# Optimization experiments

Measured on AMD Instinct MI355X. Metric: run time of the kernel, lower is better.

## Reference

```python
import jax, jax.numpy as jnp
from jax import lax
import numpy as np

RADIUS = 1
DILATION = 2
NUM_BINS = 16  # DualSimilarityLoss uses num_bins=16
ALPHA = 5.0
BETA = 0.1
NOISE = 1e-4


def _avg_pool2(x):
    b, c, h, w = x.shape
    return x.reshape(b, c, h // 2, 2, w // 2, 2).mean(axis=(3, 5))


def _conv_rep(x, k, pad):
    # replicate-pad then VALID conv, NCHW / OIHW
    xp = jnp.pad(x, ((0, 0), (0, 0), (pad, pad), (pad, pad)), mode='edge')
    return lax.conv_general_dilated(xp, k, (1, 1), 'VALID',
                                    dimension_numbers=('NCHW', 'OIHW', 'NCHW'))


def _upsample_align_corners(x, H, W):
    # bilinear, align_corners=True (matches F.interpolate(..., align_corners=True))
    b, c, h, w = x.shape

    def coords(n_out, n_in):
        pos = jnp.arange(n_out, dtype=x.dtype) * ((n_in - 1) / (n_out - 1))
        i0 = jnp.clip(jnp.floor(pos).astype(jnp.int32), 0, n_in - 2)
        return i0, pos - i0.astype(x.dtype)

    y0, fy = coords(H, h)
    x0, fx = coords(W, w)
    rows = x[:, :, y0, :] * (1.0 - fy)[None, None, :, None] \
         + x[:, :, y0 + 1, :] * fy[None, None, :, None]
    out = rows[:, :, :, x0] * (1.0 - fx) + rows[:, :, :, x0 + 1] * fx
    return out


def _compute_mind(img, key):
    B, _, H, W = img.shape
    img = _avg_pool2(img)                      # (B,1,H/2,W/2)
    img = img + NOISE * jax.random.normal(key, img.shape, img.dtype)
    h, w = img.shape[2], img.shape[3]
    pad = RADIUS * DILATION                    # 2
    k = 2 * RADIUS + 1                         # 3
    ones_k = jnp.ones((1, 1, k, k), img.dtype)
    padded = jnp.pad(img, ((0, 0), (0, 0), (pad, pad), (pad, pad)), mode='edge')
    patch_mean = lax.conv_general_dilated(padded, ones_k, (1, 1), 'VALID',
                                          dimension_numbers=('NCHW', 'OIHW', 'NCHW')) / (k * k)
    patch_mean = jnp.pad(patch_mean, ((0, 0), (0, 0), (pad, pad), (pad, pad)), mode='edge')
    c = pad
    center = padded[:, :, c:c + h, c:c + w]
    variance = (center - patch_mean[:, :, c:c + h, c:c + w]) ** 2
    variance = _conv_rep(variance, ones_k, RADIUS) / (k * k)
    variance = jnp.maximum(variance, 1e-4)
    descs = []
    for i in range(-RADIUS, RADIUS + 1):
        for j in range(-RADIUS, RADIUS + 1):
            if i == 0 and j == 0:
                continue
            dx, dy = i * DILATION, j * DILATION
            off = padded[:, :, c + dy:c + dy + h, c + dx:c + dx + w]
            diff = jnp.clip((center - off) ** 2 / (variance * 2 + 1e-6), 0.0, 50.0)
            descs.append(diff)
    m = jnp.exp(-jnp.concatenate(descs, axis=1))          # (B,8,h,w)
    m = m / (m.sum(axis=1, keepdims=True) + 1e-8)
    m = jnp.where(jnp.isnan(m), 0.0, m)
    if (h, w) != (H, W):
        m = _upsample_align_corners(m, H, W)
    return m


def _nmi_loss(x, y, kx, ky):
    B = x.shape[0]
    x = x[:, :, ::2, ::2]
    y = y[:, :, ::2, ::2]
    x = x + NOISE * jax.random.normal(kx, x.shape, x.dtype)
    y = y + NOISE * jax.random.normal(ky, y.shape, y.dtype)
    xf = jnp.clip((x.reshape(B, -1) + 1.0) / 2.0, 0.001, 0.999)
    yf = jnp.clip((y.reshape(B, -1) + 1.0) / 2.0, 0.001, 0.999)
    grid = jnp.linspace(0.0, 1.0, NUM_BINS + 1)
    xb = jnp.clip(jnp.searchsorted(grid, xf, side='left') - 1, 0, NUM_BINS - 1)
    yb = jnp.clip(jnp.searchsorted(grid, yf, side='left') - 1, 0, NUM_BINS - 1)
    idx = xb * NUM_BINS + yb                               # (B,N)
    hist = jnp.zeros((B, NUM_BINS * NUM_BINS), jnp.float32)
    hist = hist.at[jnp.arange(B)[:, None], idx].add(1.0)
    hist = hist.reshape(B, NUM_BINS, NUM_BINS)
    hist = hist / (hist.sum(axis=(1, 2), keepdims=True) + 1e-10)
    xh = hist.sum(axis=2)
    yh = hist.sum(axis=1)
    eps = 1e-5
    hist = hist + eps
    xh = xh + eps
    yh = yh + eps
    mi = jnp.sum(hist * (jnp.log(hist) - jnp.log(xh[:, :, None] * yh[:, None, :])), axis=(1, 2))
    hx = -jnp.sum(xh * jnp.log(xh), axis=1)
    hy = -jnp.sum(yh * jnp.log(yh), axis=1)
    se = hx + hy
    nmi = jnp.where(se < 1e-10, 0.0, 2.0 * mi / se)
    nmi = jnp.clip(nmi, -1.0, 1.0)
    return -jnp.clip(nmi.mean(), -1.0, 1.0)


def _reg_loss(flow, ku, kv):
    sx = jnp.array([[-1, 0, 1], [-2, 0, 2], [-1, 0, 1]], jnp.float32).reshape(1, 1, 3, 3)
    sy = jnp.array([[-1, -2, -1], [0, 0, 0], [1, 2, 1]], jnp.float32).reshape(1, 1, 3, 3)
    lp = jnp.array([[0, 1, 0], [1, -4, 1], [0, 1, 0]], jnp.float32).reshape(1, 1, 3, 3)
    f = _avg_pool2(flow)
    u = f[:, 0:1] + NOISE * jax.random.normal(ku, f[:, 0:1].shape, f.dtype)
    v = f[:, 1:2] + NOISE * jax.random.normal(kv, f[:, 1:2].shape, f.dtype)
    grad_mag = _conv_rep(u, sx, 1) ** 2 + _conv_rep(u, sy, 1) ** 2 \
             + _conv_rep(v, sx, 1) ** 2 + _conv_rep(v, sy, 1) ** 2
    lap_mag = _conv_rep(u, lp, 1) ** 2 + _conv_rep(v, lp, 1) ** 2
    return jnp.clip(grad_mag, 0.0, 100.0).mean() + jnp.clip(lap_mag, 0.0, 100.0).mean()


def _total_loss(fixed, moved, flow):
    fixed = jnp.where(jnp.isnan(fixed), 0.0, fixed)
    moved = jnp.where(jnp.isnan(moved), 0.0, moved)
    flow = jnp.where(jnp.isnan(flow), 0.0, flow)
    ks = jax.random.split(jax.random.key(42), 6)
    mi = _nmi_loss(fixed, moved, ks[0], ks[1])
    mx = _compute_mind(fixed, ks[2])
    my = _compute_mind(moved, ks[3])
    d = jnp.abs(mx - my)
    mind = jnp.where(jnp.isnan(d), 0.0, d).mean()
    reg = _reg_loss(flow, ks[4], ks[5])
    return mi + ALPHA * mind + BETA * reg


def setup_inputs() -> dict:
    key = jax.random.key(0)
    k1, k2, k3 = jax.random.split(key, 3)
    B, H, W = 8, 512, 512
    return {
        'fixed': jax.random.normal(k1, (B, 1, H, W), jnp.float32),
        'moved': jax.random.normal(k2, (B, 1, H, W), jnp.float32),
        'flow': jax.random.normal(k3, (B, 2, H, W), jnp.float32),
    }


def reference(fixed, moved, flow):
    return _total_loss(fixed, moved, flow)
```

## Files before the change

### kernel.cpp

```cpp
#include <hip/hip_runtime.h>
#include <cmath>

#define BATCH 8
#define HF 512
#define WF 512
#define HS 256
#define WS 256
#define PLANE_S (HS * WS)
#define PLANE_F (HF * WF)

#define NMIND_BLOCKS 512
#define NREG_BLOCKS  128

#define OFF_HISTP 0
#define OFF_PMIND (512 * 1024)
#define OFF_PGRAD (OFF_PMIND + NMIND_BLOCKS * 8)
#define OFF_PLAP  (OFF_PGRAD + NREG_BLOCKS * 8)
#define OFF_NMI   (OFF_PLAP + NREG_BLOCKS * 8)

#define IMG_R 39
#define IMG_S 41
#define T_R 36
#define T_S 37
#define V_R 34
#define V_S 35

__device__ __forceinline__ int clampi(int v, int lo, int hi) {
    return v < lo ? lo : (v > hi ? hi : v);
}

__device__ __forceinline__ int bin_of(float x) {
    float v = (x + 1.0f) * 0.5f;
    v = fminf(fmaxf(v, 0.001f), 0.999f);
    float t = v * 16.0f;
    float ft = floorf(t);
    int c = (int)ft + ((t > ft) ? 1 : 0);
    int b = c - 1;
    return b < 0 ? 0 : (b > 15 ? 15 : b);
}

__global__ __launch_bounds__(256, 2) void mega_mind_kernel(
    const float* __restrict__ fixed, const float* __restrict__ moved,
    unsigned* __restrict__ hist_part, double* __restrict__ pmind)
{
    const float FS = (float)(255.0 / 511.0);
    int tx = blockIdx.x, ty = blockIdx.y, b = blockIdx.z;
    int Xb = tx * 64, Yb = ty * 64;
    int dbx = (int)((float)Xb * FS);
    int dby = (int)((float)Yb * FS);
    int ibx = dbx - 3, iby = dby - 3;

    __shared__ float S[15098];
    float* imgF = S;
    float* imgM = S + IMG_R * IMG_S;
    float* varF = S + 2 * IMG_R * IMG_S;
    float* varM = varF + V_R * V_S;
    float* diff = varM + V_R * V_S;
    float* tF   = diff;
    float* tM   = diff + T_R * T_S;
    __shared__ unsigned lh[256];
    __shared__ float red[256];

    int tid = threadIdx.x;
    lh[tid] = 0u;
    __syncthreads();

    const float* fb = fixed + (size_t)b * PLANE_F;
    const float* mb = moved + (size_t)b * PLANE_F;
    int oy0 = ty * 32, ox0 = tx * 32;
    for (int i = tid; i < IMG_R * IMG_R; i += 256) {
        int r = i / IMG_R, c = i - r * IMG_R;
        int gy = iby + r, gx = ibx + c;
        int cy = clampi(gy, 0, HS - 1), cx = clampi(gx, 0, WS - 1);
        const float* fp = fb + (size_t)(cy * 2) * WF + (size_t)(cx * 2);
        const float* mp = mb + (size_t)(cy * 2) * WF + (size_t)(cx * 2);
        float2 f0 = *(const float2*)fp;
        float2 f1 = *(const float2*)(fp + WF);
        float2 m0 = *(const float2*)mp;
        float2 m1 = *(const float2*)(mp + WF);
        imgF[r * IMG_S + c] = (f0.x + f0.y + f1.x + f1.y) * 0.25f;
        imgM[r * IMG_S + c] = (m0.x + m0.y + m1.x + m1.y) * 0.25f;
        if ((unsigned)(gy - oy0) < 32u && (unsigned)(gx - ox0) < 32u) {
            atomicAdd(&lh[bin_of(f0.x) * 16 + bin_of(m0.x)], 1u);
        }
    }
    __syncthreads();
    hist_part[((size_t)(b * 64 + ty * 8 + tx)) * 256 + tid] = lh[tid];

    for (int i = tid; i < T_R * T_R; i += 256) {
        int r = i / T_R, c = i - r * T_R;
        float sF = 0.f, sM = 0.f;
        #pragma unroll
        for (int dy = 0; dy < 3; dy++)
            #pragma unroll
            for (int dx = 0; dx < 3; dx++) {
                sF += imgF[(r + dy) * IMG_S + c + dx];
                sM += imgM[(r + dy) * IMG_S + c + dx];
            }
        float dF = imgF[(r + 2) * IMG_S + c + 2] - sF / 9.0f;
        float dM = imgM[(r + 2) * IMG_S + c + 2] - sM / 9.0f;
        tF[r * T_S + c] = dF * dF;
        tM[r * T_S + c] = dM * dM;
    }
    __syncthreads();

    for (int i = tid; i < V_R * V_R; i += 256) {
        int r = i / V_R, c = i - r * V_R;
        float sF = 0.f, sM = 0.f;
        #pragma unroll
        for (int dy = 0; dy < 3; dy++)
            #pragma unroll
            for (int dx = 0; dx < 3; dx++) {
                sF += tF[(r + dy) * T_S + c + dx];
                sM += tM[(r + dy) * T_S + c + dx];
            }
        varF[r * V_S + c] = fmaxf(sF / 9.0f, 1e-4f);
        varM[r * V_S + c] = fmaxf(sM / 9.0f, 1e-4f);
    }
    __syncthreads();

    for (int i = tid; i < V_R * V_R; i += 256) {
        int r = i / V_R, c = i - r * V_R;
        float cF = imgF[(r + 3) * IMG_S + c + 3];
        float cM = imgM[(r + 3) * IMG_S + c + 3];
        float dF2 = 2.f * varF[r * V_S + c] + 1e-6f;
        float dM2 = 2.f * varM[r * V_S + c] + 1e-6f;
        float eF[8], eM[8];
        float sF = 0.f, sM = 0.f;
        int ch = 0;
        #pragma unroll
        for (int ii = -1; ii <= 1; ii++) {
            #pragma unroll
            for (int jj = -1; jj <= 1; jj++) {
                if (ii == 0 && jj == 0) continue;
                float aF = cF - imgF[(r + 3 + 2 * jj) * IMG_S + (c + 3 + 2 * ii)];
                float aM = cM - imgM[(r + 3 + 2 * jj) * IMG_S + (c + 3 + 2 * ii)];
                float qF = fminf(aF * aF / dF2, 50.f);
                float qM = fminf(aM * aM / dM2, 50.f);
                float vF_ = expf(-qF), vM_ = expf(-qM);
                eF[ch] = vF_; eM[ch] = vM_;
                sF += vF_; sM += vM_;
                ch++;
            }
        }
        float wF = 1.f / (sF + 1e-8f);
        float wM = 1.f / (sM + 1e-8f);
        float* dp = diff + (size_t)(r * V_S + c) * 8;
        #pragma unroll
        for (int q = 0; q < 8; q++) dp[q] = eF[q] * wF - eM[q] * wM;
    }
    __syncthreads();

    float local = 0.f;
    for (int k = tid; k < 64 * 64; k += 256) {
        int dy = k >> 6, dx = k & 63;
        float py = (float)(Yb + dy) * FS;
        int y0 = (int)py; if (y0 > HS - 2) y0 = HS - 2;
        float fy = py - (float)y0;
        float px = (float)(Xb + dx) * FS;
        int x0 = (int)px; if (x0 > WS - 2) x0 = WS - 2;
        float fx = px - (float)x0;
        const float* p00 = diff + (size_t)((y0 - dby) * V_S + (x0 - dbx)) * 8;
        const float* p10 = p00 + V_S * 8;
        #pragma unroll
        for (int q = 0; q < 8; q++) {
            float a  = p00[q]     * (1.f - fy) + p10[q]     * fy;
            float c2 = p00[q + 8] * (1.f - fy) + p10[q + 8] * fy;
            local += fabsf(a * (1.f - fx) + c2 * fx);
        }
    }
    red[tid] = local;
    __syncthreads();
    for (int s = 128; s > 0; s >>= 1) { if (tid < s) red[tid] += red[tid + s]; __syncthreads(); }
    if (tid == 0) pmind[b * 64 + ty * 8 + tx] = (double)red[0];
}

#define RP 66
#define RS 67
__global__ __launch_bounds__(256, 2) void reg_fused_kernel(
    const float* __restrict__ flow, double* __restrict__ pgrad, double* __restrict__ plap)
{
    int tt = blockIdx.x;
    int b = blockIdx.y;
    int tyr = tt >> 2, txr = tt & 3;
    int y0p = tyr * 64, x0p = txr * 64;
    __shared__ float U[RP * RS], V[RP * RS];
    __shared__ float red[256];
    const float* ur = flow + (size_t)(b * 2) * PLANE_F;
    const float* vr = ur + PLANE_F;
    int tid = threadIdx.x;
    for (int i = tid; i < RP * RP; i += 256) {
        int r = i / RP, c = i - r * RP;
        int gy = clampi(y0p - 1 + r, 0, HS - 1);
        int gx = clampi(x0p - 1 + c, 0, WS - 1);
        const float* uu = ur + (size_t)(gy * 2) * WF + (size_t)(gx * 2);
        const float* vv = vr + (size_t)(gy * 2) * WF + (size_t)(gx * 2);
        float2 u0 = *(const float2*)uu, u1 = *(const float2*)(uu + WF);
        float2 v0 = *(const float2*)vv, v1 = *(const float2*)(vv + WF);
        U[r * RS + c] = (u0.x + u0.y + u1.x + u1.y) * 0.25f;
        V[r * RS + c] = (v0.x + v0.y + v1.x + v1.y) * 0.25f;
    }
    __syncthreads();
    float g = 0.f, l = 0.f;
    for (int k = tid; k < 64 * 64; k += 256) {
        int y = k >> 6, x = k & 63;
        const float* u0 = &U[y * RS + x];
        const float* v0 = &V[y * RS + x];
        float a00 = u0[0],      a01 = u0[1],          a02 = u0[2];
        float a10 = u0[RS],     a11 = u0[RS + 1],     a12 = u0[RS + 2];
        float a20 = u0[2 * RS], a21 = u0[2 * RS + 1], a22 = u0[2 * RS + 2];
        float c00 = v0[0],      c01 = v0[1],          c02 = v0[2];
        float c10 = v0[RS],     c11 = v0[RS + 1],     c12 = v0[RS + 2];
        float c20 = v0[2 * RS], c21 = v0[2 * RS + 1], c22 = v0[2 * RS + 2];
        float gxu = (a02 - a00) + 2.f * (a12 - a10) + (a22 - a20);
        float gyu = (a20 - a00) + 2.f * (a21 - a01) + (a22 - a02);
        float gxv = (c02 - c00) + 2.f * (c12 - c10) + (c22 - c20);
        float gyv = (c20 - c00) + 2.f * (c21 - c01) + (c22 - c02);
        float lpu = a01 + a10 - 4.f * a11 + a12 + a21;
        float lpv = c01 + c10 - 4.f * c11 + c12 + c21;
        float grad = gxu * gxu + gyu * gyu + gxv * gxv + gyv * gyv;
        float lap = lpu * lpu + lpv * lpv;
        g += fminf(grad, 100.f);
        l += fminf(lap, 100.f);
    }
    red[tid] = g;
    __syncthreads();
    for (int s = 128; s > 0; s >>= 1) { if (tid < s) red[tid] += red[tid + s]; __syncthreads(); }
    if (tid == 0) pgrad[b * 16 + tt] = (double)red[0];
    __syncthreads();
    red[tid] = l;
    __syncthreads();
    for (int s = 128; s > 0; s >>= 1) { if (tid < s) red[tid] += red[tid + s]; __syncthreads(); }
    if (tid == 0) plap[b * 16 + tt] = (double)red[0];
}

__global__ void nmi_kernel(const unsigned* __restrict__ hist_part, float* __restrict__ nmi_out) {
    int b = blockIdx.x;
    int t = threadIdx.x;
    __shared__ float p[256];
    __shared__ float xh[16], yh[16];
    __shared__ float red[256];
    unsigned hv = 0;
    const unsigned* hp = hist_part + (size_t)b * 64 * 256 + t;
    for (int i = 0; i < 64; i++) hv += hp[i * 256];
    float pv = (float)hv / 65536.0f;
    p[t] = pv;
    __syncthreads();
    if (t < 16) {
        float s = 0.f;
        for (int j = 0; j < 16; j++) s += p[t * 16 + j];
        xh[t] = s;
    } else if (t < 32) {
        int j = t - 16;
        float s = 0.f;
        for (int i = 0; i < 16; i++) s += p[i * 16 + j];
        yh[j] = s;
    }
    __syncthreads();
    const float eps = 1e-5f;
    int i = t >> 4, j = t & 15;
    float h = pv + eps;
    float mi_term = h * (logf(h) - logf((xh[i] + eps) * (yh[j] + eps)));
    red[t] = mi_term;
    __syncthreads();
    for (int s = 128; s > 0; s >>= 1) { if (t < s) red[t] += red[t + s]; __syncthreads(); }
    float mi = red[0];
    __syncthreads();
    float e_term = 0.f;
    if (t < 16) { float xe = xh[t] + eps; e_term = -xe * logf(xe); }
    else if (t < 32) { float ye = yh[t - 16] + eps; e_term = -ye * logf(ye); }
    red[t] = e_term;
    __syncthreads();
    for (int s = 128; s > 0; s >>= 1) { if (t < s) red[t] += red[t + s]; __syncthreads(); }
    if (t == 0) {
        float se = red[0];
        float nmi = (se < 1e-10f) ? 0.f : 2.f * mi / se;
        nmi_out[b] = fminf(fmaxf(nmi, -1.f), 1.f);
    }
}

__global__ void final_kernel(const float* __restrict__ nmi, const double* __restrict__ pmind,
                             const double* __restrict__ pgrad, const double* __restrict__ plap,
                             float* __restrict__ out) {
    __shared__ double red[256];
    int t = threadIdx.x;
    double sm = 0.0;
    for (int i = t; i < NMIND_BLOCKS; i += 256) sm += pmind[i];
    double sg = 0.0, sl = 0.0;
    for (int i = t; i < NREG_BLOCKS; i += 256) { sg += pgrad[i]; sl += plap[i]; }
    red[t] = sm;
    __syncthreads();
    for (int s = 128; s > 0; s >>= 1) { if (t < s) red[t] += red[t + s]; __syncthreads(); }
    double mind_sum = red[0];
    __syncthreads();
    red[t] = sg;
    __syncthreads();
    for (int s = 128; s > 0; s >>= 1) { if (t < s) red[t] += red[t + s]; __syncthreads(); }
    double grad_sum = red[0];
    __syncthreads();
    red[t] = sl;
    __syncthreads();
    for (int s = 128; s > 0; s >>= 1) { if (t < s) red[t] += red[t + s]; __syncthreads(); }
    double lap_sum = red[0];
    if (t == 0) {
        float s = 0.f;
        for (int b = 0; b < BATCH; b++) s += nmi[b];
        s /= (float)BATCH;
        s = fminf(fmaxf(s, -1.f), 1.f);
        double mi_loss = -(double)s;
        double mind_mean = mind_sum / (64.0 * (double)PLANE_F);
        double reg = grad_sum / (double)(BATCH * PLANE_S) + lap_sum / (double)(BATCH * PLANE_S);
        out[0] = (float)(mi_loss + 5.0 * mind_mean + 0.1 * reg);
    }
}

extern "C" void kernel_launch(void* const* d_in, const int* in_sizes, int n_in,
                              void* d_out, int out_size, void* d_ws, size_t ws_size,
                              hipStream_t stream) {
    const float* fixed = (const float*)d_in[0];
    const float* moved = (const float*)d_in[1];
    const float* flow  = (const float*)d_in[2];
    float* out = (float*)d_out;
    char* ws = (char*)d_ws;

    unsigned* hist_part = (unsigned*)(ws + OFF_HISTP);
    double*   pmind     = (double*)(ws + OFF_PMIND);
    double*   pgrad     = (double*)(ws + OFF_PGRAD);
    double*   plap      = (double*)(ws + OFF_PLAP);
    float*    nmi       = (float*)(ws + OFF_NMI);

    mega_mind_kernel<<<dim3(8, 8, 8), 256, 0, stream>>>(fixed, moved, hist_part, pmind);
    reg_fused_kernel<<<dim3(16, 8), 256, 0, stream>>>(flow, pgrad, plap);
    nmi_kernel<<<BATCH, 256, 0, stream>>>(hist_part, nmi);
    final_kernel<<<1, 256, 0, stream>>>(nmi, pmind, pgrad, plap, out);
}
```

Measured before the change: 115.1 us.

## Merge MIND and regularizer kernels into one launch, fuse NMI with final reduction

Runs the regularizer blocks and the MIND/histogram blocks as one grid, picking the role by block index, so the two independent workloads share the GPU at once instead of running as back-to-back launches. The per-batch NMI kernel is folded into the single-block final reduction, which loops over the batches serially. Four launches become two, cutting launch gaps and tail idle time. The cost is that the NMI work now runs in one block rather than eight in parallel.

After: 130.3 us. +13.2%, slower.

```diff
diff --git a/kernel.cpp b/kernel.cpp
--- a/kernel.cpp
+++ b/kernel.cpp
@@ -16,7 +16,6 @@
 #define OFF_PMIND (512 * 1024)
 #define OFF_PGRAD (OFF_PMIND + NMIND_BLOCKS * 8)
 #define OFF_PLAP  (OFF_PGRAD + NREG_BLOCKS * 8)
-#define OFF_NMI   (OFF_PLAP + NREG_BLOCKS * 8)
 
 #define IMG_R 39
 #define IMG_S 41
@@ -24,6 +23,9 @@
 #define T_S 37
 #define V_R 34
 #define V_S 35
+
+#define RP 66
+#define RS 67
 
 __device__ __forceinline__ int clampi(int v, int lo, int hi) {
     return v < lo ? lo : (v > hi ? hi : v);
@@ -39,18 +41,80 @@
     return b < 0 ? 0 : (b > 15 ? 15 : b);
 }
 
-__global__ __launch_bounds__(256, 2) void mega_mind_kernel(
+__global__ __launch_bounds__(256, 2) void fused_main_kernel(
     const float* __restrict__ fixed, const float* __restrict__ moved,
-    unsigned* __restrict__ hist_part, double* __restrict__ pmind)
+    const float* __restrict__ flow,
+    unsigned* __restrict__ hist_part, double* __restrict__ pmind,
+    double* __restrict__ pgrad, double* __restrict__ plap)
 {
+    __shared__ float S[15098];
+    __shared__ unsigned lh[256];
+    __shared__ float red[256];
+    int tid = threadIdx.x;
+
+    if (blockIdx.x < NREG_BLOCKS) {
+        int rb = blockIdx.x;
+        int b = rb >> 4, tt = rb & 15;
+        int tyr = tt >> 2, txr = tt & 3;
+        int y0p = tyr * 64, x0p = txr * 64;
+        float* U = S;
+        float* V = S + RP * RS;
+        const float* ur = flow + (size_t)(b * 2) * PLANE_F;
+        const float* vr = ur + PLANE_F;
+        for (int i = tid; i < RP * RP; i += 256) {
+            int r = i / RP, c = i - r * RP;
+            int gy = clampi(y0p - 1 + r, 0, HS - 1);
+            int gx = clampi(x0p - 1 + c, 0, WS - 1);
+            const float* uu = ur + (size_t)(gy * 2) * WF + (size_t)(gx * 2);
+            const float* vv = vr + (size_t)(gy * 2) * WF + (size_t)(gx * 2);
+            float2 u0 = *(const float2*)uu, u1 = *(const float2*)(uu + WF);
+            float2 v0 = *(const float2*)vv, v1 = *(const float2*)(vv + WF);
+            U[r * RS + c] = (u0.x + u0.y + u1.x + u1.y) * 0.25f;
+            V[r * RS + c] = (v0.x + v0.y + v1.x + v1.y) * 0.25f;
+        }
+        __syncthreads();
+        float g = 0.f, l = 0.f;
+        for (int k = tid; k < 64 * 64; k += 256) {
+            int y = k >> 6, x = k & 63;
+            const float* u0 = &U[y * RS + x];
+            const float* v0 = &V[y * RS + x];
+            float a00 = u0[0],      a01 = u0[1],          a02 = u0[2];
+            float a10 = u0[RS],     a11 = u0[RS + 1],     a12 = u0[RS + 2];
+            float a20 = u0[2 * RS], a21 = u0[2 * RS + 1], a22 = u0[2 * RS + 2];
+            float c00 = v0[0],      c01 = v0[1],          c02 = v0[2];
+            float c10 = v0[RS],     c11 = v0[RS + 1],     c12 = v0[RS + 2];
+            float c20 = v0[2 * RS], c21 = v0[2 * RS + 1], c22 = v0[2 * RS + 2];
+            float gxu = (a02 - a00) + 2.f * (a12 - a10) + (a22 - a20);
+            float gyu = (a20 - a00) + 2.f * (a21 - a01) + (a22 - a02);
+            float gxv = (c02 - c00) + 2.f * (c12 - c10) + (c22 - c20);
+            float gyv = (c20 - c00) + 2.f * (c21 - c01) + (c22 - c02);
+            float lpu = a01 + a10 - 4.f * a11 + a12 + a21;
+            float lpv = c01 + c10 - 4.f * c11 + c12 + c21;
+            float grad = gxu * gxu + gyu * gyu + gxv * gxv + gyv * gyv;
+            float lap = lpu * lpu + lpv * lpv;
+            g += fminf(grad, 100.f);
+            l += fminf(lap, 100.f);
+        }
+        red[tid] = g;
+        __syncthreads();
+        for (int s = 128; s > 0; s >>= 1) { if (tid < s) red[tid] += red[tid + s]; __syncthreads(); }
+        if (tid == 0) pgrad[rb] = (double)red[0];
+        __syncthreads();
+        red[tid] = l;
+        __syncthreads();
+        for (int s = 128; s > 0; s >>= 1) { if (tid < s) red[tid] += red[tid + s]; __syncthreads(); }
+        if (tid == 0) plap[rb] = (double)red[0];
+        return;
+    }
+
+    int mb = blockIdx.x - NREG_BLOCKS;
+    int b = mb >> 6, ty = (mb >> 3) & 7, tx = mb & 7;
     const float FS = (float)(255.0 / 511.0);
-    int tx = blockIdx.x, ty = blockIdx.y, b = blockIdx.z;
     int Xb = tx * 64, Yb = ty * 64;
     int dbx = (int)((float)Xb * FS);
     int dby = (int)((float)Yb * FS);
     int ibx = dbx - 3, iby = dby - 3;
 
-    __shared__ float S[15098];
     float* imgF = S;
     float* imgM = S + IMG_R * IMG_S;
     float* varF = S + 2 * IMG_R * IMG_S;
@@ -58,22 +122,19 @@
     float* diff = varM + V_R * V_S;
     float* tF   = diff;
     float* tM   = diff + T_R * T_S;
-    __shared__ unsigned lh[256];
-    __shared__ float red[256];
-
-    int tid = threadIdx.x;
+
     lh[tid] = 0u;
     __syncthreads();
 
     const float* fb = fixed + (size_t)b * PLANE_F;
-    const float* mb = moved + (size_t)b * PLANE_F;
+    const float* mbp = moved + (size_t)b * PLANE_F;
     int oy0 = ty * 32, ox0 = tx * 32;
     for (int i = tid; i < IMG_R * IMG_R; i += 256) {
         int r = i / IMG_R, c = i - r * IMG_R;
         int gy = iby + r, gx = ibx + c;
         int cy = clampi(gy, 0, HS - 1), cx = clampi(gx, 0, WS - 1);
         const float* fp = fb + (size_t)(cy * 2) * WF + (size_t)(cx * 2);
-        const float* mp = mb + (size_t)(cy * 2) * WF + (size_t)(cx * 2);
+        const float* mp = mbp + (size_t)(cy * 2) * WF + (size_t)(cx * 2);
         float2 f0 = *(const float2*)fp;
         float2 f1 = *(const float2*)(fp + WF);
         float2 m0 = *(const float2*)mp;
@@ -85,7 +146,7 @@
         }
     }
     __syncthreads();
-    hist_part[((size_t)(b * 64 + ty * 8 + tx)) * 256 + tid] = lh[tid];
+    hist_part[(size_t)mb * 256 + tid] = lh[tid];
 
     for (int i = tid; i < T_R * T_R; i += 256) {
         int r = i / T_R, c = i - r * T_R;
@@ -172,140 +233,84 @@
     red[tid] = local;
     __syncthreads();
     for (int s = 128; s > 0; s >>= 1) { if (tid < s) red[tid] += red[tid + s]; __syncthreads(); }
-    if (tid == 0) pmind[b * 64 + ty * 8 + tx] = (double)red[0];
-}
-
-#define RP 66
-#define RS 67
-__global__ __launch_bounds__(256, 2) void reg_fused_kernel(
-    const float* __restrict__ flow, double* __restrict__ pgrad, double* __restrict__ plap)
-{
-    int tt = blockIdx.x;
-    int b = blockIdx.y;
-    int tyr = tt >> 2, txr = tt & 3;
-    int y0p = tyr * 64, x0p = txr * 64;
-    __shared__ float U[RP * RS], V[RP * RS];
-    __shared__ float red[256];
-    const float* ur = flow + (size_t)(b * 2) * PLANE_F;
-    const float* vr = ur + PLANE_F;
-    int tid = threadIdx.x;
-    for (int i = tid; i < RP * RP; i += 256) {
-        int r = i / RP, c = i - r * RP;
-        int gy = clampi(y0p - 1 + r, 0, HS - 1);
-        int gx = clampi(x0p - 1 + c, 0, WS - 1);
-        const float* uu = ur + (size_t)(gy * 2) * WF + (size_t)(gx * 2);
-        const float* vv = vr + (size_t)(gy * 2) * WF + (size_t)(gx * 2);
-        float2 u0 = *(const float2*)uu, u1 = *(const float2*)(uu + WF);
-        float2 v0 = *(const float2*)vv, v1 = *(const float2*)(vv + WF);
-        U[r * RS + c] = (u0.x + u0.y + u1.x + u1.y) * 0.25f;
-        V[r * RS + c] = (v0.x + v0.y + v1.x + v1.y) * 0.25f;
-    }
-    __syncthreads();
-    float g = 0.f, l = 0.f;
-    for (int k = tid; k < 64 * 64; k += 256) {
-        int y = k >> 6, x = k & 63;
-        const float* u0 = &U[y * RS + x];
-        const float* v0 = &V[y * RS + x];
-        float a00 = u0[0],      a01 = u0[1],          a02 = u0[2];
-        float a10 = u0[RS],     a11 = u0[RS + 1],     a12 = u0[RS + 2];
-        float a20 = u0[2 * RS], a21 = u0[2 * RS + 1], a22 = u0[2 * RS + 2];
-        float c00 = v0[0],      c01 = v0[1],          c02 = v0[2];
-        float c10 = v0[RS],     c11 = v0[RS + 1],     c12 = v0[RS + 2];
-        float c20 = v0[2 * RS], c21 = v0[2 * RS + 1], c22 = v0[2 * RS + 2];
-        float gxu = (a02 - a00) + 2.f * (a12 - a10) + (a22 - a20);
-        float gyu = (a20 - a00) + 2.f * (a21 - a01) + (a22 - a02);
-        float gxv = (c02 - c00) + 2.f * (c12 - c10) + (c22 - c20);
-        float gyv = (c20 - c00) + 2.f * (c21 - c01) + (c22 - c02);
-        float lpu = a01 + a10 - 4.f * a11 + a12 + a21;
-        float lpv = c01 + c10 - 4.f * c11 + c12 + c21;
-        float grad = gxu * gxu + gyu * gyu + gxv * gxv + gyv * gyv;
-        float lap = lpu * lpu + lpv * lpv;
-        g += fminf(grad, 100.f);
-        l += fminf(lap, 100.f);
-    }
-    red[tid] = g;
-    __syncthreads();
-    for (int s = 128; s > 0; s >>= 1) { if (tid < s) red[tid] += red[tid + s]; __syncthreads(); }
-    if (tid == 0) pgrad[b * 16 + tt] = (double)red[0];
-    __syncthreads();
-    red[tid] = l;
-    __syncthreads();
-    for (int s = 128; s > 0; s >>= 1) { if (tid < s) red[tid] += red[tid + s]; __syncthreads(); }
-    if (tid == 0) plap[b * 16 + tt] = (double)red[0];
-}
-
-__global__ void nmi_kernel(const unsigned* __restrict__ hist_part, float* __restrict__ nmi_out) {
-    int b = blockIdx.x;
+    if (tid == 0) pmind[mb] = (double)red[0];
+}
+
+__global__ void nmi_final_kernel(const unsigned* __restrict__ hist_part,
+                                 const double* __restrict__ pmind,
+                                 const double* __restrict__ pgrad,
+                                 const double* __restrict__ plap,
+                                 float* __restrict__ out) {
     int t = threadIdx.x;
     __shared__ float p[256];
     __shared__ float xh[16], yh[16];
     __shared__ float red[256];
-    unsigned hv = 0;
-    const unsigned* hp = hist_part + (size_t)b * 64 * 256 + t;
-    for (int i = 0; i < 64; i++) hv += hp[i * 256];
-    float pv = (float)hv / 65536.0f;
-    p[t] = pv;
-    __syncthreads();
-    if (t < 16) {
-        float s = 0.f;
-        for (int j = 0; j < 16; j++) s += p[t * 16 + j];
-        xh[t] = s;
-    } else if (t < 32) {
-        int j = t - 16;
-        float s = 0.f;
-        for (int i = 0; i < 16; i++) s += p[i * 16 + j];
-        yh[j] = s;
-    }
-    __syncthreads();
-    const float eps = 1e-5f;
-    int i = t >> 4, j = t & 15;
-    float h = pv + eps;
-    float mi_term = h * (logf(h) - logf((xh[i] + eps) * (yh[j] + eps)));
-    red[t] = mi_term;
-    __syncthreads();
-    for (int s = 128; s > 0; s >>= 1) { if (t < s) red[t] += red[t + s]; __syncthreads(); }
-    float mi = red[0];
-    __syncthreads();
-    float e_term = 0.f;
-    if (t < 16) { float xe = xh[t] + eps; e_term = -xe * logf(xe); }
-    else if (t < 32) { float ye = yh[t - 16] + eps; e_term = -ye * logf(ye); }
-    red[t] = e_term;
-    __syncthreads();
-    for (int s = 128; s > 0; s >>= 1) { if (t < s) red[t] += red[t + s]; __syncthreads(); }
-    if (t == 0) {
-        float se = red[0];
-        float nmi = (se < 1e-10f) ? 0.f : 2.f * mi / se;
-        nmi_out[b] = fminf(fmaxf(nmi, -1.f), 1.f);
-    }
-}
-
-__global__ void final_kernel(const float* __restrict__ nmi, const double* __restrict__ pmind,
-                             const double* __restrict__ pgrad, const double* __restrict__ plap,
-                             float* __restrict__ out) {
-    __shared__ double red[256];
-    int t = threadIdx.x;
+    __shared__ double redd[256];
+    __shared__ float nmi_acc_s;
+    if (t == 0) nmi_acc_s = 0.f;
+    __syncthreads();
+
+    for (int b = 0; b < BATCH; b++) {
+        unsigned hv = 0;
+        const unsigned* hp = hist_part + (size_t)b * 64 * 256 + t;
+        for (int i = 0; i < 64; i++) hv += hp[i * 256];
+        float pv = (float)hv / 65536.0f;
+        p[t] = pv;
+        __syncthreads();
+        if (t < 16) {
+            float s = 0.f;
+            for (int j = 0; j < 16; j++) s += p[t * 16 + j];
+            xh[t] = s;
+        } else if (t < 32) {
+            int j = t - 16;
+            float s = 0.f;
+            for (int i = 0; i < 16; i++) s += p[i * 16 + j];
+            yh[j] = s;
+        }
+        __syncthreads();
+        const float eps = 1e-5f;
+        int i = t >> 4, j = t & 15;
+        float h = pv + eps;
+        float mi_term = h * (logf(h) - logf((xh[i] + eps) * (yh[j] + eps)));
+        red[t] = mi_term;
+        __syncthreads();
+        for (int s = 128; s > 0; s >>= 1) { if (t < s) red[t] += red[t + s]; __syncthreads(); }
+        float mi = red[0];
+        __syncthreads();
+        float e_term = 0.f;
+        if (t < 16) { float xe = xh[t] + eps; e_term = -xe * logf(xe); }
+        else if (t < 32) { float ye = yh[t - 16] + eps; e_term = -ye * logf(ye); }
+        red[t] = e_term;
+        __syncthreads();
+        for (int s = 128; s > 0; s >>= 1) { if (t < s) red[t] += red[t + s]; __syncthreads(); }
+        if (t == 0) {
+            float se = red[0];
+            float nmi = (se < 1e-10f) ? 0.f : 2.f * mi / se;
+            nmi_acc_s += fminf(fmaxf(nmi, -1.f), 1.f);
+        }
+        __syncthreads();
+    }
+
     double sm = 0.0;
     for (int i = t; i < NMIND_BLOCKS; i += 256) sm += pmind[i];
     double sg = 0.0, sl = 0.0;
     for (int i = t; i < NREG_BLOCKS; i += 256) { sg += pgrad[i]; sl += plap[i]; }
-    red[t] = sm;
-    __syncthreads();
-    for (int s = 128; s > 0; s >>= 1) { if (t < s) red[t] += red[t + s]; __syncthreads(); }
-    double mind_sum = red[0];
-    __syncthreads();
-    red[t] = sg;
-    __syncthreads();
-    for (int s = 128; s > 0; s >>= 1) { if (t < s) red[t] += red[t + s]; __syncthreads(); }
-    double grad_sum = red[0];
-    __syncthreads();
-    red[t] = sl;
-    __syncthreads();
-    for (int s = 128; s > 0; s >>= 1) { if (t < s) red[t] += red[t + s]; __syncthreads(); }
-    double lap_sum = red[0];
+    redd[t] = sm;
+    __syncthreads();
+    for (int s = 128; s > 0; s >>= 1) { if (t < s) redd[t] += redd[t + s]; __syncthreads(); }
+    double mind_sum = redd[0];
+    __syncthreads();
+    redd[t] = sg;
+    __syncthreads();
+    for (int s = 128; s > 0; s >>= 1) { if (t < s) redd[t] += redd[t + s]; __syncthreads(); }
+    double grad_sum = redd[0];
+    __syncthreads();
+    redd[t] = sl;
+    __syncthreads();
+    for (int s = 128; s > 0; s >>= 1) { if (t < s) redd[t] += redd[t + s]; __syncthreads(); }
+    double lap_sum = redd[0];
     if (t == 0) {
-        float s = 0.f;
-        for (int b = 0; b < BATCH; b++) s += nmi[b];
-        s /= (float)BATCH;
+        float s = nmi_acc_s / (float)BATCH;
         s = fminf(fmaxf(s, -1.f), 1.f);
         double mi_loss = -(double)s;
         double mind_mean = mind_sum / (64.0 * (double)PLANE_F);
@@ -327,10 +332,8 @@
     double*   pmind     = (double*)(ws + OFF_PMIND);
     double*   pgrad     = (double*)(ws + OFF_PGRAD);
     double*   plap      = (double*)(ws + OFF_PLAP);
-    float*    nmi       = (float*)(ws + OFF_NMI);
-
-    mega_mind_kernel<<<dim3(8, 8, 8), 256, 0, stream>>>(fixed, moved, hist_part, pmind);
-    reg_fused_kernel<<<dim3(16, 8), 256, 0, stream>>>(flow, pgrad, plap);
-    nmi_kernel<<<BATCH, 256, 0, stream>>>(hist_part, nmi);
-    final_kernel<<<1, 256, 0, stream>>>(nmi, pmind, pgrad, plap, out);
-}
+
+    fused_main_kernel<<<NREG_BLOCKS + NMIND_BLOCKS, 256, 0, stream>>>(
+        fixed, moved, flow, hist_part, pmind, pgrad, plap);
+    nmi_final_kernel<<<1, 256, 0, stream>>>(hist_part, pmind, pgrad, plap, out);
+}
```
